# Performance work log

Hardware: AMD Instinct MI355X
Metric: run time of the kernel (lower is better)

## Reference

```python
import jax, jax.numpy as jnp
import numpy as np

N_NODES = 50000
N_EDGES = 800000
IN_DIM = 128
HID = 64
HEADS = 4
EDGE_DIM = 3
NEG_SLOPE = 0.2  # PyG GATv2 default


def setup_inputs() -> dict:
    key = jax.random.key(0)
    ks = jax.random.split(key, 16)
    def glorot(k, shape):
        fan_in = shape[0]
        return (jax.random.normal(k, shape, jnp.float32) / jnp.sqrt(jnp.float32(fan_in)))
    x = jax.random.normal(ks[0], (N_NODES, IN_DIM), jnp.float32)
    edge_attr = jax.random.normal(ks[1], (N_EDGES, EDGE_DIM), jnp.float32)
    edge_index = jax.random.randint(ks[2], (2, N_EDGES), 0, N_NODES, jnp.int32)
    # layer 1: GATv2Conv(IN_DIM -> HID, heads=HEADS, edge_dim=3, concat=True)
    W1l = glorot(ks[3], (IN_DIM, HEADS * HID))
    W1r = glorot(ks[4], (IN_DIM, HEADS * HID))
    W1e = glorot(ks[5], (EDGE_DIM, HEADS * HID))
    att1 = glorot(ks[6], (HEADS, HID))
    b1 = jnp.zeros((HEADS * HID,), jnp.float32)
    # layer 2: GATv2Conv(HEADS*HID -> 1, heads=1, edge_dim=3, concat=False)
    W2l = glorot(ks[7], (HEADS * HID, 1))
    W2r = glorot(ks[8], (HEADS * HID, 1))
    W2e = glorot(ks[9], (EDGE_DIM, 1))
    att2 = glorot(ks[10], (1, 1))
    b2 = jnp.zeros((1,), jnp.float32)
    return {"x": x, "edge_attr": edge_attr, "W1l": W1l, "W1r": W1r, "W1e": W1e,
            "att1": att1, "b1": b1, "W2l": W2l, "W2r": W2r, "W2e": W2e,
            "att2": att2, "b2": b2, "edge_index": edge_index}


def _add_self_loops(edge_index, edge_attr, n_nodes):
    # PyG GATv2Conv add_self_loops=True with fill_value='mean' for edge_attr
    loops = jnp.arange(n_nodes, dtype=edge_index.dtype)
    ei = jnp.concatenate([edge_index, jnp.stack([loops, loops])], axis=1)
    loop_attr = jnp.broadcast_to(edge_attr.mean(axis=0, keepdims=True),
                                 (n_nodes, edge_attr.shape[1]))
    ea = jnp.concatenate([edge_attr, loop_attr], axis=0)
    return ei, ea


def _gatv2(x, edge_index, edge_attr, Wl, Wr, We, att, bias, heads, concat):
    n = x.shape[0]
    c = Wl.shape[1] // heads
    src, dst = edge_index[0], edge_index[1]
    xl = (x @ Wl).reshape(n, heads, c)   # source-side transform
    xr = (x @ Wr).reshape(n, heads, c)   # target-side transform
    ef = (edge_attr @ We).reshape(-1, heads, c)
    m = jax.nn.leaky_relu(xl[src] + xr[dst] + ef, NEG_SLOPE)   # [E,H,C]
    logits = jnp.einsum('ehc,hc->eh', m, att)                  # [E,H]
    mx = jax.ops.segment_max(logits, dst, num_segments=n)      # segment softmax over dst
    a = jnp.exp(logits - mx[dst])
    denom = jax.ops.segment_sum(a, dst, num_segments=n)
    alpha = a / denom[dst]                                     # [E,H]
    out = jax.ops.segment_sum(xl[src] * alpha[:, :, None], dst, num_segments=n)  # [N,H,C]
    out = out.reshape(n, heads * c) if concat else out.mean(axis=1)
    return out + bias


def reference(x, edge_attr, W1l, W1r, W1e, att1, b1, W2l, W2r, W2e, att2, b2, edge_index):
    n = x.shape[0]
    ei, ea = _add_self_loops(edge_index, edge_attr, n)
    h = _gatv2(x, ei, ea, W1l, W1r, W1e, att1, b1, HEADS, True)
    h = jax.nn.elu(h)  # dropout identity in eval mode
    gat_scores = _gatv2(h, ei, ea, W2l, W2r, W2e, att2, b2, 1, False).squeeze(-1)
    portfolio_weights = jax.nn.softmax(gat_scores, axis=0)
    return portfolio_weights, gat_scores
```

## Files before the change

kernel.cpp:

```cpp
#include <hip/hip_runtime.h>
#include <hip/hip_bf16.h>
#include <hip/hip_fp16.h>

typedef __attribute__((ext_vector_type(8))) short short8;
typedef __attribute__((ext_vector_type(4))) float floatx4;
typedef _Float16 h2 __attribute__((ext_vector_type(2)));
typedef _Float16 h4 __attribute__((ext_vector_type(4)));
typedef _Float16 h8 __attribute__((ext_vector_type(8)));
typedef __fp16 fp16x2 __attribute__((ext_vector_type(2)));

#define N_NODESC 50000
#define MPAD     50016
#define N_EDGESC 800000
#define E_TOTC   850000
#define IN_DIMC  128
#define FDIM     256
#define HEADSC   4
#define HIDC     64
#define NEG_SLOPE 0.2f
#define RESCALE_THR 8.0f

#define SCAN_TILE 1024
#define SCAN_NB   ((N_NODESC + SCAN_TILE - 1) / SCAN_TILE)

__device__ __forceinline__ float wave_sum(float v){
  #pragma unroll
  for (int m = 32; m > 0; m >>= 1) v += __shfl_xor(v, m, 64);
  return v;
}
__device__ __forceinline__ float wave_max(float v){
  #pragma unroll
  for (int m = 32; m > 0; m >>= 1) v = fmaxf(v, __shfl_xor(v, m, 64));
  return v;
}
__device__ __forceinline__ float g16_sum(float v){
  #pragma unroll
  for (int m = 8; m > 0; m >>= 1) v += __shfl_xor(v, m, 64);
  return v;
}
__device__ __forceinline__ float g16_max(float v){
  #pragma unroll
  for (int m = 8; m > 0; m >>= 1) v = fmaxf(v, __shfl_xor(v, m, 64));
  return v;
}

__device__ __forceinline__ h2 f2h2(float v){
  return __builtin_bit_cast(h2, __builtin_amdgcn_cvt_pkrtz(v, v));
}
__device__ __forceinline__ float fdot2(h2 a, h2 b, float c){
  return __builtin_amdgcn_fdot2(__builtin_bit_cast(fp16x2, a),
                                __builtin_bit_cast(fp16x2, b), c, false);
}

__global__ __launch_bounds__(256) void k_mean(const float* __restrict__ ea,
                                              float* __restrict__ meanacc){
  float s0 = 0.f, s1 = 0.f, s2 = 0.f;
  for (int i = blockIdx.x * blockDim.x + threadIdx.x; i < N_EDGESC;
       i += gridDim.x * blockDim.x){
    s0 += ea[i*3+0]; s1 += ea[i*3+1]; s2 += ea[i*3+2];
  }
  s0 = wave_sum(s0); s1 = wave_sum(s1); s2 = wave_sum(s2);
  __shared__ float red[3][4];
  int lane = threadIdx.x & 63, w = threadIdx.x >> 6;
  if (lane == 0){ red[0][w] = s0; red[1][w] = s1; red[2][w] = s2; }
  __syncthreads();
  if (threadIdx.x == 0){
    float t0 = 0.f, t1 = 0.f, t2 = 0.f;
    for (int i = 0; i < 4; i++){ t0 += red[0][i]; t1 += red[1][i]; t2 += red[2][i]; }
    atomicAdd(&meanacc[0], t0); atomicAdd(&meanacc[1], t1); atomicAdd(&meanacc[2], t2);
  }
}

__global__ __launch_bounds__(256) void k_count(const int* __restrict__ ei,
                                               int* __restrict__ deg,
                                               int* __restrict__ rank){
  int e = blockIdx.x * blockDim.x + threadIdx.x;
  if (e >= N_EDGESC) return;
  rank[e] = atomicAdd(&deg[ei[N_EDGESC + e]], 1);
}

__global__ __launch_bounds__(256) void k_cvtx(const float* __restrict__ x,
                                              _Float16* __restrict__ xb){
  size_t tid = (size_t)blockIdx.x * 256 + threadIdx.x;
  size_t base = tid * 4;
  const size_t NELEM = (size_t)N_NODESC * IN_DIMC;
  h4 o;
  if (base + 3 < NELEM){
    const float4* xp = (const float4*)(x + base);
    float4 v = *xp;
    o[0] = (_Float16)v.x; o[1] = (_Float16)v.y;
    o[2] = (_Float16)v.z; o[3] = (_Float16)v.w;
  } else {
    #pragma unroll
    for (int f = 0; f < 4; f++){
      size_t i = base + f;
      float v = (i < NELEM) ? x[i] : 0.f;
      o[f] = (_Float16)v;
    }
  }
  *(h4*)(xb + base) = o;
}

__global__ __launch_bounds__(256) void k_cvtw(const float* __restrict__ W1l,
                                              const float* __restrict__ W1r,
                                              _Float16* __restrict__ Bfrag){
  int idx = blockIdx.x * 256 + threadIdx.x;
  int mat = idx >> 15;
  int r   = idx & 32767;
  int k   = r >> 8, n = r & 255;
  float v = mat ? W1r[r] : W1l[r];
  int pos = (mat << 15) + (((k >> 3) << 8) + n) * 8 + (k & 7);
  Bfrag[pos] = (_Float16)v;
}

__global__ __launch_bounds__(256) void k_gemm_mfma(const _Float16* __restrict__ xb,
                                                   const _Float16* __restrict__ Bfrag,
                                                   _Float16* __restrict__ xl,
                                                   _Float16* __restrict__ xr){
  const int mat = blockIdx.y;
  const int r0  = blockIdx.x * 32;
  const int w = threadIdx.x >> 6, lane = threadIdx.x & 63;
  const int quad = lane >> 4, l16 = lane & 15;
  const _Float16* Bm = Bfrag + ((size_t)mat << 15);
  _Float16* C = mat ? xr : xl;

  h8 afr[2][4];
  #pragma unroll
  for (int ms = 0; ms < 2; ms++)
    #pragma unroll
    for (int ks = 0; ks < 4; ks++){
      const _Float16* p = xb + (size_t)(r0 + ms*16 + l16) * IN_DIMC + ks*32 + quad*8;
      afr[ms][ks] = *reinterpret_cast<const h8*>(p);
    }
  const int n0 = w * 64;
  floatx4 acc[2][4];
  #pragma unroll
  for (int ms = 0; ms < 2; ms++)
    #pragma unroll
    for (int ns = 0; ns < 4; ns++){
      floatx4 z = {0.f, 0.f, 0.f, 0.f};
      acc[ms][ns] = z;
    }
  #pragma unroll
  for (int ks = 0; ks < 4; ks++){
    #pragma unroll
    for (int ns = 0; ns < 4; ns++){
      int n = n0 + ns*16 + l16;
      int kblk = ks*4 + quad;
      h8 bfr = *reinterpret_cast<const h8*>(Bm + ((size_t)kblk*256 + n)*8);
      acc[0][ns] = __builtin_amdgcn_mfma_f32_16x16x32_f16(afr[0][ks], bfr, acc[0][ns], 0, 0, 0);
      acc[1][ns] = __builtin_amdgcn_mfma_f32_16x16x32_f16(afr[1][ks], bfr, acc[1][ns], 0, 0, 0);
    }
  }
  #pragma unroll
  for (int ms = 0; ms < 2; ms++)
    #pragma unroll
    for (int ns = 0; ns < 4; ns++){
      int col = n0 + ns*16 + l16;
      #pragma unroll
      for (int rg = 0; rg < 4; rg++){
        int row = r0 + ms*16 + quad*4 + rg;
        C[(size_t)row * FDIM + col] = (_Float16)acc[ms][ns][rg];
      }
    }
}

__global__ __launch_bounds__(256) void k_scan_pa(const int* __restrict__ deg,
                                                 int* __restrict__ pre,
                                                 int* __restrict__ bsum){
  int b = blockIdx.x, t = threadIdx.x;
  int lane = t & 63, w = t >> 6;
  int base = b * SCAN_TILE + t * 4;
  int4 v = {0, 0, 0, 0};
  if (base + 3 < N_NODESC){
    v = *(const int4*)(deg + base);
    v.x += 1; v.y += 1; v.z += 1; v.w += 1;
  } else {
    if (base + 0 < N_NODESC) v.x = deg[base + 0] + 1;
    if (base + 1 < N_NODESC) v.y = deg[base + 1] + 1;
    if (base + 2 < N_NODESC) v.z = deg[base + 2] + 1;
    if (base + 3 < N_NODESC) v.w = deg[base + 3] + 1;
  }
  int s = v.x + v.y + v.z + v.w;
  int inc = s;
  #pragma unroll
  for (int off = 1; off < 64; off <<= 1){
    int u = __shfl_up(inc, off, 64);
    if (lane >= off) inc += u;
  }
  __shared__ int wsum[4];
  if (lane == 63) wsum[w] = inc;
  __syncthreads();
  int wadd = 0;
  #pragma unroll
  for (int i = 0; i < 4; i++) if (i < w) wadd += wsum[i];
  int excl = inc - s + wadd;
  if (base + 3 < N_NODESC){
    int4 o;
    o.x = excl; o.y = o.x + v.x; o.z = o.y + v.y; o.w = o.z + v.z;
    *(int4*)(pre + base) = o;
  } else {
    int run = excl;
    if (base + 0 < N_NODESC){ pre[base + 0] = run; run += v.x; }
    if (base + 1 < N_NODESC){ pre[base + 1] = run; run += v.y; }
    if (base + 2 < N_NODESC){ pre[base + 2] = run; run += v.z; }
    if (base + 3 < N_NODESC){ pre[base + 3] = run; }
  }
  if (t == 255) bsum[b] = wsum[0] + wsum[1] + wsum[2] + wsum[3];
}

__global__ __launch_bounds__(64) void k_scan_pb(const int* __restrict__ bsum,
                                                int* __restrict__ boff,
                                                int* __restrict__ offsets){
  int lane = threadIdx.x;
  int s = (lane < SCAN_NB) ? bsum[lane] : 0;
  int inc = s;
  #pragma unroll
  for (int off = 1; off < 64; off <<= 1){
    int u = __shfl_up(inc, off, 64);
    if (lane >= off) inc += u;
  }
  if (lane < SCAN_NB) boff[lane] = inc - s;
  if (lane == 63) offsets[N_NODESC] = inc;
}

__global__ __launch_bounds__(256) void k_scan_pc(const int* __restrict__ pre,
                                                 const int* __restrict__ boff,
                                                 int* __restrict__ offsets){
  int b = blockIdx.x;
  int base = b * SCAN_TILE + threadIdx.x * 4;
  int add = boff[b];
  if (base + 3 < N_NODESC){
    int4 p = *(const int4*)(pre + base);
    p.x += add; p.y += add; p.z += add; p.w += add;
    *(int4*)(offsets + base) = p;
  } else {
    #pragma unroll
    for (int f = 0; f < 4; f++){
      int i = base + f;
      if (i < N_NODESC) offsets[i] = pre[i] + add;
    }
  }
}

__global__ __launch_bounds__(256) void k_scatter(const int* __restrict__ ei,
                                                 const float* __restrict__ ea,
                                                 const float* __restrict__ meanacc,
                                                 const int* __restrict__ offsets,
                                                 const int* __restrict__ rank,
                                                 float4* __restrict__ rec){
  int e = blockIdx.x * blockDim.x + threadIdx.x;
  if (e >= E_TOTC) return;
  int pos; float4 r;
  if (e < N_EDGESC){
    int src = ei[e], dst = ei[N_EDGESC + e];
    r.x = __int_as_float(src);
    r.y = ea[e*3+0]; r.z = ea[e*3+1]; r.w = ea[e*3+2];
    pos = offsets[dst] + rank[e];
  } else {
    int i = e - N_EDGESC;
    const float inv = 1.0f / (float)N_EDGESC;
    r.x = __int_as_float(i);
    r.y = meanacc[0]*inv; r.z = meanacc[1]*inv; r.w = meanacc[2]*inv;
    pos = offsets[i + 1] - 1;
  }
  rec[pos] = r;
}

__global__ __launch_bounds__(256, 4) void k_attn1(const int* __restrict__ offsets,
                                                  const float4* __restrict__ rec,
                                                  const _Float16* __restrict__ xl,
                                                  const _Float16* __restrict__ xr,
                                                  const float* __restrict__ W1e,
                                                  const float* __restrict__ att1,
                                                  const float* __restrict__ b1,
                                                  const float* __restrict__ W2l,
                                                  const float* __restrict__ W2r,
                                                  float* __restrict__ sl,
                                                  float* __restrict__ sr){
  const int t = threadIdx.x, lane = t & 63, w = t >> 6;
  const int n = blockIdx.x * 4 + w;
  const int half = lane >> 5, l32 = lane & 31;
  const int f0 = l32 * 8;

  h2 xrp[4], w0p[4], w1p[4], w2p[4], atp[4];
  {
    h8 xw = *(const h8*)(xr + (size_t)n * FDIM + f0);
    #pragma unroll
    for (int k = 0; k < 4; k++) xrp[k] = h2{xw[2*k], xw[2*k+1]};
    float4 a0 = *(const float4*)(W1e + f0);
    float4 a1 = *(const float4*)(W1e + f0 + 4);
    w0p[0]=h2{(_Float16)a0.x,(_Float16)a0.y}; w0p[1]=h2{(_Float16)a0.z,(_Float16)a0.w};
    w0p[2]=h2{(_Float16)a1.x,(_Float16)a1.y}; w0p[3]=h2{(_Float16)a1.z,(_Float16)a1.w};
    float4 b0 = *(const float4*)(W1e + FDIM + f0);
    float4 b4 = *(const float4*)(W1e + FDIM + f0 + 4);
    w1p[0]=h2{(_Float16)b0.x,(_Float16)b0.y}; w1p[1]=h2{(_Float16)b0.z,(_Float16)b0.w};
    w1p[2]=h2{(_Float16)b4.x,(_Float16)b4.y}; w1p[3]=h2{(_Float16)b4.z,(_Float16)b4.w};
    float4 c0 = *(const float4*)(W1e + 2*FDIM + f0);
    float4 c4 = *(const float4*)(W1e + 2*FDIM + f0 + 4);
    w2p[0]=h2{(_Float16)c0.x,(_Float16)c0.y}; w2p[1]=h2{(_Float16)c0.z,(_Float16)c0.w};
    w2p[2]=h2{(_Float16)c4.x,(_Float16)c4.y}; w2p[3]=h2{(_Float16)c4.z,(_Float16)c4.w};
    float4 d0 = *(const float4*)(att1 + f0);
    float4 d4 = *(const float4*)(att1 + f0 + 4);
    atp[0]=h2{(_Float16)d0.x,(_Float16)d0.y}; atp[1]=h2{(_Float16)d0.z,(_Float16)d0.w};
    atp[2]=h2{(_Float16)d4.x,(_Float16)d4.y}; atp[3]=h2{(_Float16)d4.z,(_Float16)d4.w};
  }
  const h2 nsl2 = h2{(_Float16)NEG_SLOPE, (_Float16)NEG_SLOPE};
  const int beg = offsets[n], end = offsets[n + 1];
  const int last = end - 1;

  float m = -1e30f, den = 0.f;
  float acc[8] = {0.f,0.f,0.f,0.f,0.f,0.f,0.f,0.f};

  int j = beg + half;
  float4 rc  = rec[min(j, last)];
  float4 rcn = rec[min(j + 2, last)];
  unsigned off0 = ((unsigned)__float_as_int(rc.x) << 8) + f0;
  h8 raw = *(const h8*)(xl + off0);

  for (; j < end; j += 2){
    unsigned offn = ((unsigned)__float_as_int(rcn.x) << 8) + f0;
    h8 rawn = *(const h8*)(xl + offn);
    const float e0 = rc.y, e1 = rc.z, e2 = rc.w;
    rc = rcn;
    rcn = rec[min(j + 4, last)];

    h2 he0 = f2h2(e0), he1 = f2h2(e1), he2 = f2h2(e2);
    float pp = 0.f;
    #pragma unroll
    for (int k = 0; k < 4; k++){
      h2 xk = h2{raw[2*k], raw[2*k+1]};
      h2 v = xk + xrp[k] + he0*w0p[k] + he1*w1p[k] + he2*w2p[k];
      v = __builtin_elementwise_max(v, nsl2 * v);
      pp = fdot2(v, atp[k], pp);
    }
    pp += __shfl_xor(pp, 1, 64);
    pp += __shfl_xor(pp, 2, 64);
    pp += __shfl_xor(pp, 4, 64);

    if (pp > m + RESCALE_THR){
      float corr = __expf(m - pp);
      den *= corr;
      #pragma unroll
      for (int k = 0; k < 8; k++) acc[k] *= corr;
      m = pp;
    }
    float al = __expf(pp - m);
    den += al;
    #pragma unroll
    for (int k = 0; k < 8; k++) acc[k] = fmaf((float)raw[k], al, acc[k]);

    raw = rawn;
  }

  float m_o   = __shfl_xor(m, 32, 64);
  float den_o = __shfl_xor(den, 32, 64);
  float m_t = fmaxf(m, m_o);
  float sc   = __expf(m - m_t);
  float sc_o = __expf(m_o - m_t);
  float den_t = den * sc + den_o * sc_o;
  float invd = 1.0f / den_t;

  float4 bb0 = *(const float4*)(b1 + f0);
  float4 bb4 = *(const float4*)(b1 + f0 + 4);
  float bb[8] = {bb0.x,bb0.y,bb0.z,bb0.w,bb4.x,bb4.y,bb4.z,bb4.w};
  float hv[8];
  #pragma unroll
  for (int k = 0; k < 8; k++){
    float a_o = __shfl_xor(acc[k], 32, 64);
    float tot = acc[k] * sc + a_o * sc_o;
    float h = tot * invd + bb[k];
    hv[k] = (h > 0.f) ? h : (__expf(h) - 1.f);
  }
  float4 l0 = *(const float4*)(W2l + f0);
  float4 l4 = *(const float4*)(W2l + f0 + 4);
  float4 r0 = *(const float4*)(W2r + f0);
  float4 r4 = *(const float4*)(W2r + f0 + 4);
  float wl[8] = {l0.x,l0.y,l0.z,l0.w,l4.x,l4.y,l4.z,l4.w};
  float wr[8] = {r0.x,r0.y,r0.z,r0.w,r4.x,r4.y,r4.z,r4.w};
  float pa = 0.f, pb = 0.f;
  #pragma unroll
  for (int k = 0; k < 8; k++){ pa += hv[k]*wl[k]; pb += hv[k]*wr[k]; }
  #pragma unroll
  for (int msk = 16; msk > 0; msk >>= 1){
    pa += __shfl_xor(pa, msk, 64);
    pb += __shfl_xor(pb, msk, 64);
  }
  if (lane == 0){ sl[n] = pa; sr[n] = pb; }
}

__device__ __forceinline__ unsigned fkey(float f){
  unsigned u = __float_as_uint(f);
  return u ^ ((u >> 31) ? 0xFFFFFFFFu : 0x80000000u);
}
__device__ __forceinline__ float funkey(unsigned k){
  unsigned u = (k >> 31) ? (k ^ 0x80000000u) : ~k;
  return __uint_as_float(u);
}

__global__ __launch_bounds__(256) void k_attn2(const int* __restrict__ offsets,
                                               const float4* __restrict__ rec,
                                               const float* __restrict__ W2e,
                                               const float* __restrict__ att2,
                                               const float* __restrict__ b2p,
                                               const float* __restrict__ sl,
                                               const float* __restrict__ sr,
                                               float* __restrict__ scores,
                                               float* __restrict__ out){
  int t = threadIdx.x, l16 = t & 15;
  int n = blockIdx.x * 16 + (t >> 4);
  if (n >= N_NODESC) return;
  const float attv = att2[0];
  const float w2e0 = W2e[0], w2e1 = W2e[1], w2e2 = W2e[2];
  const float srn = sr[n];
  int beg = offsets[n], end = offsets[n + 1];
  float m = -1e30f, den = 0.f, num = 0.f;
  for (int j = beg + l16; j < end; j += 16){
    float4 rc = rec[j];
    float slv = sl[__float_as_int(rc.x)];
    float v = slv + srn + rc.y*w2e0 + rc.z*w2e1 + rc.w*w2e2;
    v = (v > 0.f) ? v : NEG_SLOPE * v;
    float lg = v * attv;
    float mn = fmaxf(m, lg);
    float corr = __expf(m - mn);
    float pe   = __expf(lg - mn);
    den = den * corr + pe;
    num = num * corr + pe * slv;
    m = mn;
  }
  float mg = g16_max(m);
  float scale = __expf(m - mg);
  float deng = g16_sum(den * scale);
  float numg = g16_sum(num * scale);
  if (l16 == 0){
    float s = numg / deng + b2p[0];
    scores[n] = s;
    out[N_NODESC + n] = s;
  }
}

__global__ __launch_bounds__(256) void k_smax_max(const float* __restrict__ scores,
                                                  unsigned* __restrict__ redmax){
  float m = -1e30f;
  for (int i = blockIdx.x * blockDim.x + threadIdx.x; i < N_NODESC;
       i += gridDim.x * blockDim.x)
    m = fmaxf(m, scores[i]);
  m = wave_max(m);
  __shared__ float ws_[4];
  int lane = threadIdx.x & 63, w = threadIdx.x >> 6;
  if (lane == 0) ws_[w] = m;
  __syncthreads();
  if (threadIdx.x == 0){
    for (int i = 1; i < 4; i++) m = fmaxf(m, ws_[i]);
    atomicMax(redmax, fkey(m));
  }
}

__global__ __launch_bounds__(256) void k_smax_sum(const float* __restrict__ scores,
                                                  const unsigned* __restrict__ redmax,
                                                  float* __restrict__ redsum){
  float mx = funkey(*redmax);
  float s = 0.f;
  for (int i = blockIdx.x * blockDim.x + threadIdx.x; i < N_NODESC;
       i += gridDim.x * blockDim.x)
    s += __expf(scores[i] - mx);
  s = wave_sum(s);
  __shared__ float ws_[4];
  int lane = threadIdx.x & 63, w = threadIdx.x >> 6;
  if (lane == 0) ws_[w] = s;
  __syncthreads();
  if (threadIdx.x == 0){
    float t = 0.f;
    for (int i = 0; i < 4; i++) t += ws_[i];
    atomicAdd(redsum, t);
  }
}

__global__ __launch_bounds__(256) void k_smax_write(const float* __restrict__ scores,
                                                    const unsigned* __restrict__ redmax,
                                                    const float* __restrict__ redsum,
                                                    float* __restrict__ out){
  int i = blockIdx.x * blockDim.x + threadIdx.x;
  if (i >= N_NODESC) return;
  float mx = funkey(*redmax);
  float inv = 1.0f / (*redsum);
  out[i] = __expf(scores[i] - mx) * inv;
}

extern "C" void kernel_launch(void* const* d_in, const int* in_sizes, int n_in,
                              void* d_out, int out_size, void* d_ws, size_t ws_size,
                              hipStream_t stream) {
  const float* x    = (const float*)d_in[0];
  const float* ea   = (const float*)d_in[1];
  const float* W1l  = (const float*)d_in[2];
  const float* W1r  = (const float*)d_in[3];
  const float* W1e  = (const float*)d_in[4];
  const float* att1 = (const float*)d_in[5];
  const float* b1   = (const float*)d_in[6];
  const float* W2l  = (const float*)d_in[7];
  const float* W2r  = (const float*)d_in[8];
  const float* W2e  = (const float*)d_in[9];
  const float* att2 = (const float*)d_in[10];
  const float* b2   = (const float*)d_in[11];
  const int*   ei   = (const int*)d_in[12];
  float* out = (float*)d_out;

  char* w = (char*)d_ws;
  size_t off = 0;
  auto alloc = [&](size_t bytes) -> char* {
    char* p = w + off;
    off = (off + bytes + 255) & ~(size_t)255;
    return p;
  };
  float*    meanacc = (float*)alloc(16);
  unsigned* redmax  = (unsigned*)alloc(8);
  float*    redsum  = (float*)((char*)redmax + 4);
  int*      deg     = (int*)alloc((size_t)N_NODESC * 4);
  size_t zero_bytes = off;
  int*   offsets = (int*)alloc((size_t)(N_NODESC + 1) * 4);
  int*   rank    = (int*)alloc((size_t)N_EDGESC * 4);
  int*   pre     = (int*)alloc((size_t)N_NODESC * 4);
  int*   bsum    = (int*)alloc((size_t)SCAN_NB * 4);
  int*   boff    = (int*)alloc((size_t)SCAN_NB * 4);
  float4* rec    = (float4*)alloc((size_t)E_TOTC * 16);
  float* sl      = (float*)alloc((size_t)N_NODESC * 4);
  float* sr      = (float*)alloc((size_t)N_NODESC * 4);
  float* scores  = (float*)alloc((size_t)N_NODESC * 4);
  _Float16* xb    = (_Float16*)alloc((size_t)MPAD * IN_DIMC * 2);
  _Float16* Bfrag = (_Float16*)alloc((size_t)2 * 128 * 256 * 2);
  _Float16* xl    = (_Float16*)alloc((size_t)MPAD * FDIM * 2);
  _Float16* xr    = (_Float16*)alloc((size_t)MPAD * FDIM * 2);
  (void)ws_size; (void)in_sizes; (void)n_in; (void)out_size;

  hipMemsetAsync(d_ws, 0, zero_bytes, stream);

  k_mean  <<<400, 256, 0, stream>>>(ea, meanacc);
  k_count <<<(N_EDGESC + 255) / 256, 256, 0, stream>>>(ei, deg, rank);
  k_cvtx  <<<(int)(((size_t)MPAD * IN_DIMC / 4 + 255) / 256), 256, 0, stream>>>(x, xb);
  k_cvtw  <<<256, 256, 0, stream>>>(W1l, W1r, Bfrag);
  k_scan_pa<<<SCAN_NB, 256, 0, stream>>>(deg, pre, bsum);
  k_scan_pb<<<1, 64, 0, stream>>>(bsum, boff, offsets);
  k_scan_pc<<<SCAN_NB, 256, 0, stream>>>(pre, boff, offsets);
  k_scatter<<<(E_TOTC + 255) / 256, 256, 0, stream>>>(ei, ea, meanacc, offsets,
                                                      rank, rec);
  {
    dim3 g(MPAD / 32, 2);
    k_gemm_mfma<<<g, 256, 0, stream>>>(xb, Bfrag, xl, xr);
  }
  k_attn1 <<<N_NODESC / 4, 256, 0, stream>>>(offsets, rec, xl, xr,
                                             W1e, att1, b1, W2l, W2r, sl, sr);
  k_attn2 <<<(N_NODESC + 15) / 16, 256, 0, stream>>>(offsets, rec, W2e, att2, b2,
                                                     sl, sr, scores, out);
  k_smax_max <<<256, 256, 0, stream>>>(scores, redmax);
  k_smax_sum <<<256, 256, 0, stream>>>(scores, redmax, redsum);
  k_smax_write<<<(N_NODESC + 255) / 256, 256, 0, stream>>>(scores, redmax, redsum, out);
}
```

Before: 302.1 us.

## Fuse prep kernels, convert x inside GEMM, merge scan passes, pre-pack edge attrs

Merges the edge-attribute mean and weight repacking into one launch, and drops the separate x-to-fp16 conversion kernel by loading fp32 x and converting inside the GEMM A-fragment load. The block-offset scan pass is folded into the final scan pass, where each block computes its own prefix with a wave reduction. Edge attributes are stored in the edge records already converted to fp16 so attention layer 1 no longer converts them per edge. These cut launches and an intermediate buffer round trip, but the GEMM now reads twice the bytes for x, and layer 2 reads fp16-rounded edge attributes.

```diff
diff --git a/kernel.cpp b/kernel.cpp
--- a/kernel.cpp
+++ b/kernel.cpp
@@ -22,12 +22,18 @@
 
 #define SCAN_TILE 1024
 #define SCAN_NB   ((N_NODESC + SCAN_TILE - 1) / SCAN_TILE)
+#define MEAN_NB   400
 
 __device__ __forceinline__ float wave_sum(float v){
   #pragma unroll
   for (int m = 32; m > 0; m >>= 1) v += __shfl_xor(v, m, 64);
   return v;
 }
+__device__ __forceinline__ int wave_sum_i(int v){
+  #pragma unroll
+  for (int m = 32; m > 0; m >>= 1) v += __shfl_xor(v, m, 64);
+  return v;
+}
 __device__ __forceinline__ float wave_max(float v){
   #pragma unroll
   for (int m = 32; m > 0; m >>= 1) v = fmaxf(v, __shfl_xor(v, m, 64));
@@ -44,30 +50,43 @@
   return v;
 }
 
-__device__ __forceinline__ h2 f2h2(float v){
-  return __builtin_bit_cast(h2, __builtin_amdgcn_cvt_pkrtz(v, v));
+__device__ __forceinline__ float f2h2_bits(float v){
+  return __builtin_bit_cast(float, __builtin_amdgcn_cvt_pkrtz(v, v));
 }
 __device__ __forceinline__ float fdot2(h2 a, h2 b, float c){
   return __builtin_amdgcn_fdot2(__builtin_bit_cast(fp16x2, a),
                                 __builtin_bit_cast(fp16x2, b), c, false);
 }
 
-__global__ __launch_bounds__(256) void k_mean(const float* __restrict__ ea,
-                                              float* __restrict__ meanacc){
-  float s0 = 0.f, s1 = 0.f, s2 = 0.f;
-  for (int i = blockIdx.x * blockDim.x + threadIdx.x; i < N_EDGESC;
-       i += gridDim.x * blockDim.x){
-    s0 += ea[i*3+0]; s1 += ea[i*3+1]; s2 += ea[i*3+2];
-  }
-  s0 = wave_sum(s0); s1 = wave_sum(s1); s2 = wave_sum(s2);
-  __shared__ float red[3][4];
-  int lane = threadIdx.x & 63, w = threadIdx.x >> 6;
-  if (lane == 0){ red[0][w] = s0; red[1][w] = s1; red[2][w] = s2; }
-  __syncthreads();
-  if (threadIdx.x == 0){
-    float t0 = 0.f, t1 = 0.f, t2 = 0.f;
-    for (int i = 0; i < 4; i++){ t0 += red[0][i]; t1 += red[1][i]; t2 += red[2][i]; }
-    atomicAdd(&meanacc[0], t0); atomicAdd(&meanacc[1], t1); atomicAdd(&meanacc[2], t2);
+__global__ __launch_bounds__(256) void k_prep(const float* __restrict__ ea,
+                                              float* __restrict__ meanacc,
+                                              const float* __restrict__ W1l,
+                                              const float* __restrict__ W1r,
+                                              _Float16* __restrict__ Bfrag){
+  int b = blockIdx.x;
+  if (b < MEAN_NB){
+    float s0 = 0.f, s1 = 0.f, s2 = 0.f;
+    for (int i = b * 256 + threadIdx.x; i < N_EDGESC; i += MEAN_NB * 256){
+      s0 += ea[i*3+0]; s1 += ea[i*3+1]; s2 += ea[i*3+2];
+    }
+    s0 = wave_sum(s0); s1 = wave_sum(s1); s2 = wave_sum(s2);
+    __shared__ float red[3][4];
+    int lane = threadIdx.x & 63, w = threadIdx.x >> 6;
+    if (lane == 0){ red[0][w] = s0; red[1][w] = s1; red[2][w] = s2; }
+    __syncthreads();
+    if (threadIdx.x == 0){
+      float t0 = 0.f, t1 = 0.f, t2 = 0.f;
+      for (int i = 0; i < 4; i++){ t0 += red[0][i]; t1 += red[1][i]; t2 += red[2][i]; }
+      atomicAdd(&meanacc[0], t0); atomicAdd(&meanacc[1], t1); atomicAdd(&meanacc[2], t2);
+    }
+  } else {
+    int idx = (b - MEAN_NB) * 256 + threadIdx.x;
+    int mat = idx >> 15;
+    int r   = idx & 32767;
+    int k   = r >> 8, n = r & 255;
+    float v = mat ? W1r[r] : W1l[r];
+    int pos = (mat << 15) + (((k >> 3) << 8) + n) * 8 + (k & 7);
+    Bfrag[pos] = (_Float16)v;
   }
 }
 
@@ -79,41 +98,7 @@
   rank[e] = atomicAdd(&deg[ei[N_EDGESC + e]], 1);
 }
 
-__global__ __launch_bounds__(256) void k_cvtx(const float* __restrict__ x,
-                                              _Float16* __restrict__ xb){
-  size_t tid = (size_t)blockIdx.x * 256 + threadIdx.x;
-  size_t base = tid * 4;
-  const size_t NELEM = (size_t)N_NODESC * IN_DIMC;
-  h4 o;
-  if (base + 3 < NELEM){
-    const float4* xp = (const float4*)(x + base);
-    float4 v = *xp;
-    o[0] = (_Float16)v.x; o[1] = (_Float16)v.y;
-    o[2] = (_Float16)v.z; o[3] = (_Float16)v.w;
-  } else {
-    #pragma unroll
-    for (int f = 0; f < 4; f++){
-      size_t i = base + f;
-      float v = (i < NELEM) ? x[i] : 0.f;
-      o[f] = (_Float16)v;
-    }
-  }
-  *(h4*)(xb + base) = o;
-}
-
-__global__ __launch_bounds__(256) void k_cvtw(const float* __restrict__ W1l,
-                                              const float* __restrict__ W1r,
-                                              _Float16* __restrict__ Bfrag){
-  int idx = blockIdx.x * 256 + threadIdx.x;
-  int mat = idx >> 15;
-  int r   = idx & 32767;
-  int k   = r >> 8, n = r & 255;
-  float v = mat ? W1r[r] : W1l[r];
-  int pos = (mat << 15) + (((k >> 3) << 8) + n) * 8 + (k & 7);
-  Bfrag[pos] = (_Float16)v;
-}
-
-__global__ __launch_bounds__(256) void k_gemm_mfma(const _Float16* __restrict__ xb,
+__global__ __launch_bounds__(256) void k_gemm_mfma(const float* __restrict__ x,
                                                    const _Float16* __restrict__ Bfrag,
                                                    _Float16* __restrict__ xl,
                                                    _Float16* __restrict__ xr){
@@ -126,12 +111,22 @@
 
   h8 afr[2][4];
   #pragma unroll
-  for (int ms = 0; ms < 2; ms++)
+  for (int ms = 0; ms < 2; ms++){
+    int row = r0 + ms*16 + l16;
+    bool ok = row < N_NODESC;
     #pragma unroll
     for (int ks = 0; ks < 4; ks++){
-      const _Float16* p = xb + (size_t)(r0 + ms*16 + l16) * IN_DIMC + ks*32 + quad*8;
-      afr[ms][ks] = *reinterpret_cast<const h8*>(p);
-    }
+      if (ok){
+        const float* p = x + (size_t)row * IN_DIMC + ks*32 + quad*8;
+        float4 v0 = *(const float4*)(p);
+        float4 v1 = *(const float4*)(p + 4);
+        afr[ms][ks] = h8{(_Float16)v0.x, (_Float16)v0.y, (_Float16)v0.z, (_Float16)v0.w,
+                         (_Float16)v1.x, (_Float16)v1.y, (_Float16)v1.z, (_Float16)v1.w};
+      } else {
+        afr[ms][ks] = h8{0,0,0,0,0,0,0,0};
+      }
+    }
+  }
   const int n0 = w * 64;
   floatx4 acc[2][4];
   #pragma unroll
@@ -209,27 +204,29 @@
   if (t == 255) bsum[b] = wsum[0] + wsum[1] + wsum[2] + wsum[3];
 }
 
-__global__ __launch_bounds__(64) void k_scan_pb(const int* __restrict__ bsum,
-                                                int* __restrict__ boff,
-                                                int* __restrict__ offsets){
-  int lane = threadIdx.x;
-  int s = (lane < SCAN_NB) ? bsum[lane] : 0;
-  int inc = s;
-  #pragma unroll
-  for (int off = 1; off < 64; off <<= 1){
-    int u = __shfl_up(inc, off, 64);
-    if (lane >= off) inc += u;
-  }
-  if (lane < SCAN_NB) boff[lane] = inc - s;
-  if (lane == 63) offsets[N_NODESC] = inc;
-}
-
 __global__ __launch_bounds__(256) void k_scan_pc(const int* __restrict__ pre,
-                                                 const int* __restrict__ boff,
+                                                 const int* __restrict__ bsum,
                                                  int* __restrict__ offsets){
   int b = blockIdx.x;
+  __shared__ int sadd;
+  if (threadIdx.x < 64){
+    int lane = threadIdx.x;
+    int v   = (lane < SCAN_NB) ? bsum[lane] : 0;
+    int pfx = (lane < b) ? v : 0;
+    pfx = wave_sum_i(pfx);
+    if (lane == 0){
+      sadd = pfx;
+      if (b == 0){
+      }
+    }
+    if (b == 0){
+      int tot = wave_sum_i(v);
+      if (lane == 0) offsets[N_NODESC] = tot;
+    }
+  }
+  __syncthreads();
+  int add = sadd;
   int base = b * SCAN_TILE + threadIdx.x * 4;
-  int add = boff[b];
   if (base + 3 < N_NODESC){
     int4 p = *(const int4*)(pre + base);
     p.x += add; p.y += add; p.z += add; p.w += add;
@@ -255,13 +252,17 @@
   if (e < N_EDGESC){
     int src = ei[e], dst = ei[N_EDGESC + e];
     r.x = __int_as_float(src);
-    r.y = ea[e*3+0]; r.z = ea[e*3+1]; r.w = ea[e*3+2];
+    r.y = f2h2_bits(ea[e*3+0]);
+    r.z = f2h2_bits(ea[e*3+1]);
+    r.w = f2h2_bits(ea[e*3+2]);
     pos = offsets[dst] + rank[e];
   } else {
     int i = e - N_EDGESC;
     const float inv = 1.0f / (float)N_EDGESC;
     r.x = __int_as_float(i);
-    r.y = meanacc[0]*inv; r.z = meanacc[1]*inv; r.w = meanacc[2]*inv;
+    r.y = f2h2_bits(meanacc[0]*inv);
+    r.z = f2h2_bits(meanacc[1]*inv);
+    r.w = f2h2_bits(meanacc[2]*inv);
     pos = offsets[i + 1] - 1;
   }
   rec[pos] = r;
@@ -321,11 +322,12 @@
   for (; j < end; j += 2){
     unsigned offn = ((unsigned)__float_as_int(rcn.x) << 8) + f0;
     h8 rawn = *(const h8*)(xl + offn);
-    const float e0 = rc.y, e1 = rc.z, e2 = rc.w;
+    h2 he0 = __builtin_bit_cast(h2, rc.y);
+    h2 he1 = __builtin_bit_cast(h2, rc.z);
+    h2 he2 = __builtin_bit_cast(h2, rc.w);
     rc = rcn;
     rcn = rec[min(j + 4, last)];
 
-    h2 he0 = f2h2(e0), he1 = f2h2(e1), he2 = f2h2(e2);
     float pp = 0.f;
     #pragma unroll
     for (int k = 0; k < 4; k++){
@@ -418,7 +420,10 @@
   for (int j = beg + l16; j < end; j += 16){
     float4 rc = rec[j];
     float slv = sl[__float_as_int(rc.x)];
-    float v = slv + srn + rc.y*w2e0 + rc.z*w2e1 + rc.w*w2e2;
+    float e0 = (float)__builtin_bit_cast(h2, rc.y)[0];
+    float e1 = (float)__builtin_bit_cast(h2, rc.z)[0];
+    float e2 = (float)__builtin_bit_cast(h2, rc.w)[0];
+    float v = slv + srn + e0*w2e0 + e1*w2e1 + e2*w2e2;
     v = (v > 0.f) ? v : NEG_SLOPE * v;
     float lg = v * attv;
     float mn = fmaxf(m, lg);
@@ -521,12 +526,10 @@
   int*   rank    = (int*)alloc((size_t)N_EDGESC * 4);
   int*   pre     = (int*)alloc((size_t)N_NODESC * 4);
   int*   bsum    = (int*)alloc((size_t)SCAN_NB * 4);
-  int*   boff    = (int*)alloc((size_t)SCAN_NB * 4);
   float4* rec    = (float4*)alloc((size_t)E_TOTC * 16);
   float* sl      = (float*)alloc((size_t)N_NODESC * 4);
   float* sr      = (float*)alloc((size_t)N_NODESC * 4);
   float* scores  = (float*)alloc((size_t)N_NODESC * 4);
-  _Float16* xb    = (_Float16*)alloc((size_t)MPAD * IN_DIMC * 2);
   _Float16* Bfrag = (_Float16*)alloc((size_t)2 * 128 * 256 * 2);
   _Float16* xl    = (_Float16*)alloc((size_t)MPAD * FDIM * 2);
   _Float16* xr    = (_Float16*)alloc((size_t)MPAD * FDIM * 2);
@@ -534,18 +537,15 @@
 
   hipMemsetAsync(d_ws, 0, zero_bytes, stream);
 
-  k_mean  <<<400, 256, 0, stream>>>(ea, meanacc);
+  k_prep  <<<MEAN_NB + 256, 256, 0, stream>>>(ea, meanacc, W1l, W1r, Bfrag);
   k_count <<<(N_EDGESC + 255) / 256, 256, 0, stream>>>(ei, deg, rank);
-  k_cvtx  <<<(int)(((size_t)MPAD * IN_DIMC / 4 + 255) / 256), 256, 0, stream>>>(x, xb);
-  k_cvtw  <<<256, 256, 0, stream>>>(W1l, W1r, Bfrag);
   k_scan_pa<<<SCAN_NB, 256, 0, stream>>>(deg, pre, bsum);
-  k_scan_pb<<<1, 64, 0, stream>>>(bsum, boff, offsets);
-  k_scan_pc<<<SCAN_NB, 256, 0, stream>>>(pre, boff, offsets);
+  k_scan_pc<<<SCAN_NB, 256, 0, stream>>>(pre, bsum, offsets);
   k_scatter<<<(E_TOTC + 255) / 256, 256, 0, stream>>>(ei, ea, meanacc, offsets,
                                                       rank, rec);
   {
     dim3 g(MPAD / 32, 2);
-    k_gemm_mfma<<<g, 256, 0, stream>>>(xb, Bfrag, xl, xr);
+    k_gemm_mfma<<<g, 256, 0, stream>>>(x, Bfrag, xl, xr);
   }
   k_attn1 <<<N_NODESC / 4, 256, 0, stream>>>(offsets, rec, xl, xr,
                                              W1e, att1, b1, W2l, W2r, sl, sr);
```

Result: no change. 305.4 us (+1.1%).
